# Kernel tuning notes

Hardware: AMD Instinct MI355X
Metric: run time of the kernel (lower is better)

The kernel has to match this reference:

```python
import jax, jax.numpy as jnp
import numpy as np

N, E, F, G, C, L = 20000, 320000, 75, 64, 10, 5
EPS = 1e-5


def setup_inputs():
    key = jax.random.key(0)
    ks = jax.random.split(key, 16)
    x = jax.random.normal(ks[0], (N, 6), jnp.float32)
    edge_index = jax.random.randint(ks[1], (2, E), 0, N, dtype=jnp.int32)
    batch = jnp.sort(jax.random.randint(ks[2], (N,), 0, G, dtype=jnp.int32))
    gcn_w = jax.random.normal(ks[3], (6, F), jnp.float32) / np.sqrt(6.0)
    gcn_b = jnp.zeros((F,), jnp.float32)
    pre_w = jax.random.normal(ks[4], (L, 2 * F, F), jnp.float32) / np.sqrt(2.0 * F)
    pre_b = jnp.zeros((L, F), jnp.float32)
    post_w = jax.random.normal(ks[5], (L, 13 * F, F), jnp.float32) / np.sqrt(13.0 * F)
    post_b = jnp.zeros((L, F), jnp.float32)
    lin_w = jax.random.normal(ks[6], (L, F, F), jnp.float32) / np.sqrt(1.0 * F)
    lin_b = jnp.zeros((L, F), jnp.float32)
    bn_g = jnp.ones((L, F), jnp.float32)
    bn_b = jnp.zeros((L, F), jnp.float32)
    w1 = jax.random.normal(ks[7], (F, 50), jnp.float32) / np.sqrt(1.0 * F)
    b1 = jnp.zeros((50,), jnp.float32)
    w2 = jax.random.normal(ks[8], (50, 25), jnp.float32) / np.sqrt(50.0)
    b2 = jnp.zeros((25,), jnp.float32)
    w3 = jax.random.normal(ks[9], (25, C), jnp.float32) / np.sqrt(25.0)
    b3 = jnp.zeros((C,), jnp.float32)
    return dict(x=x, edge_index=edge_index, batch=batch, gcn_w=gcn_w, gcn_b=gcn_b,
                pre_w=pre_w, pre_b=pre_b, post_w=post_w, post_b=post_b,
                lin_w=lin_w, lin_b=lin_b, bn_g=bn_g, bn_b=bn_b,
                w1=w1, b1=b1, w2=w2, b2=b2, w3=w3, b3=b3)


def reference(x, edge_index, batch, gcn_w, gcn_b, pre_w, pre_b, post_w, post_b,
              lin_w, lin_b, bn_g, bn_b, w1, b1, w2, b2, w3, b3):
    row, col = edge_index[0], edge_index[1]  # messages flow row (j) -> col (i)
    ones_e = jnp.ones((E,), jnp.float32)

    # ---- GCNConv(6, 75) with self-loops and symmetric normalization ----
    xw = x @ gcn_w                                   # [N, F]
    deg = jax.ops.segment_sum(ones_e, col, N) + 1.0  # in-degree + self-loop
    dinv = 1.0 / jnp.sqrt(deg)
    norm_e = (dinv[row] * dinv[col])[:, None]        # [E, 1]
    h = jax.ops.segment_sum(norm_e * xw[row], col, N) + (dinv * dinv)[:, None] * xw + gcn_b

    # ---- degree-based scalers (shared by all PNA layers) ----
    cnt = jax.ops.segment_sum(ones_e, col, N)        # in-degree per node
    avg_log = jnp.mean(jnp.log(cnt + 1.0))           # avg_deg['log'] from this graph's degree histogram
    d = jnp.maximum(cnt, 1.0)
    amp = (jnp.log(d + 1.0) / avg_log)[:, None]      # amplification
    att = (avg_log / jnp.log(d + 1.0))[:, None]      # attenuation
    cnt_c = jnp.maximum(cnt, 1.0)[:, None]
    has_nb = (cnt > 0)[:, None]

    for l in range(L):
        # pre-MLP on [x_i, x_j] per edge
        m = jnp.concatenate([h[col], h[row]], axis=-1) @ pre_w[l] + pre_b[l]  # [E, F]
        s = jax.ops.segment_sum(m, col, N)
        mean = s / cnt_c
        mean_sq = jax.ops.segment_sum(m * m, col, N) / cnt_c
        std = jnp.sqrt(jax.nn.relu(mean_sq - mean * mean) + EPS)
        mn = jnp.where(has_nb, jax.ops.segment_min(m, col, N), 0.0)
        mx = jnp.where(has_nb, jax.ops.segment_max(m, col, N), 0.0)
        agg = jnp.concatenate([mean, mn, mx, std], axis=-1)          # [N, 4F]
        scaled = jnp.concatenate([agg, agg * amp, agg * att], -1)    # [N, 12F]
        o = jnp.concatenate([h, scaled], axis=-1) @ post_w[l] + post_b[l]  # post-MLP
        o = o @ lin_w[l] + lin_b[l]                                  # final lin
        mu = o.mean(axis=0)
        var = o.var(axis=0)
        o = (o - mu) / jnp.sqrt(var + EPS) * bn_g[l] + bn_b[l]       # BatchNorm (batch stats)
        h = jax.nn.relu(o)

    # ---- global_add_pool + MLP (dropout = identity in eval) ----
    g = jax.ops.segment_sum(h, batch, G)
    g = jax.nn.relu(g @ w1 + b1)
    g = jax.nn.relu(g @ w2 + b2)
    return g @ w3 + b3  # [G, C]
```

## Files before the change

### kernel.cpp

```cpp
#include <hip/hip_runtime.h>
#include <hip/hip_bf16.h>

#define NN 20000
#define EE 320000
#define FF 75
#define GG 64
#define LL 5
#define EPS 1e-5f

#define KUV 96
#define NUV 160
#define KPOST 384
#define NPOST 240
#define KLIN 96
#define ASTR 392

typedef short bf16x8 __attribute__((ext_vector_type(8)));
typedef float f32x4 __attribute__((ext_vector_type(4)));

__device__ inline void gAtomicAdd(float* p, float v) { unsafeAtomicAdd(p, v); }

__device__ inline ushort f2bs(float x) {
    __hip_bfloat16 b = __float2bfloat16(x);
    return *(ushort*)&b;
}

__device__ inline float bs2f(ushort u) {
    unsigned int x = ((unsigned int)u) << 16;
    return __uint_as_float(x);
}


__global__ void count_kernel(const int* __restrict__ col, int* __restrict__ cnt, int E) {
    int e = blockIdx.x * blockDim.x + threadIdx.x;
    if (e < E) atomicAdd(&cnt[col[e]], 1);
}

__global__ void dinv_partial_kernel(const int* __restrict__ cnt, float* __restrict__ dinv,
                                    float* __restrict__ scal, int* __restrict__ bsum, int N) {
    __shared__ float red[256];
    __shared__ int redi[256];
    int tid = threadIdx.x;
    int i = blockIdx.x * 256 + tid;
    float lg = 0.f;
    int cv = 0;
    if (i < N) {
        cv = cnt[i];
        float c = (float)cv;
        dinv[i] = 1.f / sqrtf(c + 1.f);
        lg = logf(c + 1.f);
    }
    red[tid] = lg;
    redi[tid] = cv;
    __syncthreads();
    for (int s = 128; s > 0; s >>= 1) {
        if (tid < s) { red[tid] += red[tid + s]; redi[tid] += redi[tid + s]; }
        __syncthreads();
    }
    if (tid == 0) {
        gAtomicAdd(&scal[0], red[0]);
        bsum[blockIdx.x] = redi[0];
    }
}

__global__ void scanb_kernel(const int* __restrict__ bsum, int* __restrict__ bbase,
                             int* __restrict__ offs, int NB) {
    __shared__ int sh[128];
    int tid = threadIdx.x;
    int v = (tid < NB) ? bsum[tid] : 0;
    sh[tid] = v;
    __syncthreads();
    for (int d = 1; d < 128; d <<= 1) {
        int t = (tid >= d) ? sh[tid - d] : 0;
        __syncthreads();
        sh[tid] += t;
        __syncthreads();
    }
    if (tid < NB) bbase[tid] = sh[tid] - v;
    if (tid == 0) offs[NN] = EE;
}

__global__ void offs_kernel(const int* __restrict__ cnt, const int* __restrict__ bbase,
                            int* __restrict__ offs, int* __restrict__ cursor, int N) {
    __shared__ int sh[256];
    int tid = threadIdx.x;
    int i = blockIdx.x * 256 + tid;
    int v = (i < N) ? cnt[i] : 0;
    sh[tid] = v;
    __syncthreads();
    for (int d = 1; d < 256; d <<= 1) {
        int t = (tid >= d) ? sh[tid - d] : 0;
        __syncthreads();
        sh[tid] += t;
        __syncthreads();
    }
    int excl = sh[tid] - v + bbase[blockIdx.x];
    if (i < N) { offs[i] = excl; cursor[i] = excl; }
}

__global__ void fill_kernel(const int* __restrict__ row, const int* __restrict__ col,
                            int* __restrict__ cursor, int* __restrict__ csr, int E) {
    int e = blockIdx.x * blockDim.x + threadIdx.x;
    if (e < E) {
        int c = col[e];
        int pos = atomicAdd(&cursor[c], 1);
        csr[pos] = row[e];
    }
}


__global__ void xs_kernel(const float* __restrict__ x, const float* __restrict__ gw,
                          const float* __restrict__ dinv, ushort* __restrict__ xs, int N) {
    int idx = blockIdx.x * 256 + threadIdx.x;
    if (idx >= N * 80) return;
    int n = idx / 80, t = idx % 80;
    float v = 0.f;
    if (t < FF) {
        float acc = 0.f;
#pragma unroll
        for (int k = 0; k < 6; k++) acc += x[n * 6 + k] * gw[k * FF + t];
        v = dinv[n] * acc;
    }
    xs[idx] = f2bs(v);
}

__global__ __launch_bounds__(64) void gcn_kernel(
    const ushort* __restrict__ xs, const float* __restrict__ dinv,
    const int* __restrict__ offs, const int* __restrict__ csr,
    const float* __restrict__ gcn_b, const int* __restrict__ cnt,
    const float* __restrict__ scal, float* __restrict__ o2,
    float* __restrict__ amp, float* __restrict__ att, int N) {
    int i = blockIdx.x;
    int lane = threadIdx.x;
    int s0 = offs[i], s1 = offs[i + 1];
    if (lane < 40) {
        float a0 = 0.f, a1 = 0.f;
        int k = s0;
        for (; k + 1 < s1; k += 2) {
            int r0 = csr[k], r1 = csr[k + 1];
            ushort2 v0 = *(const ushort2*)(xs + (size_t)r0 * 80 + 2 * lane);
            ushort2 v1 = *(const ushort2*)(xs + (size_t)r1 * 80 + 2 * lane);
            a0 += bs2f(v0.x) + bs2f(v1.x);
            a1 += bs2f(v0.y) + bs2f(v1.y);
        }
        if (k < s1) {
            int r0 = csr[k];
            ushort2 v0 = *(const ushort2*)(xs + (size_t)r0 * 80 + 2 * lane);
            a0 += bs2f(v0.x);
            a1 += bs2f(v0.y);
        }
        ushort2 vs = *(const ushort2*)(xs + (size_t)i * 80 + 2 * lane);
        a0 += bs2f(vs.x);
        a1 += bs2f(vs.y);
        float di = dinv[i];
        int t0 = 2 * lane, t1 = 2 * lane + 1;
        if (t0 < FF) o2[(size_t)i * 80 + t0] = di * a0 + gcn_b[t0];
        if (t1 < FF) o2[(size_t)i * 80 + t1] = di * a1 + gcn_b[t1];
    } else if (lane == 63) {
        float al = scal[0] / (float)N;
        float d = fmaxf((float)cnt[i], 1.f);
        float lg = logf(d + 1.f);
        amp[i] = lg / al;
        att[i] = al / lg;
    }
}


#define S_UV (LL * NUV * KUV)
#define S_POST (LL * NPOST * KPOST)
#define S_LIN (LL * 80 * KLIN)

__global__ void prep_bt_kernel(const float* __restrict__ pre_w, const float* __restrict__ pre_b,
                               const float* __restrict__ post_w, const float* __restrict__ lin_w,
                               ushort* __restrict__ BTuv, ushort* __restrict__ BTpost,
                               ushort* __restrict__ BTlin) {
    int idx = blockIdx.x * 256 + threadIdx.x;
    if (idx < S_UV) {
        int l = idx / (NUV * KUV);
        int r = idx % (NUV * KUV);
        int c = r / KUV, k = r % KUV;
        float v = 0.f;
        if (k < FF) {
            if (c < FF) v = pre_w[((size_t)l * 150 + k) * FF + c];
            else if (c >= 80 && c < 80 + FF) v = pre_w[((size_t)l * 150 + FF + k) * FF + (c - 80)];
        } else if (k == FF && c < FF) {
            v = pre_b[l * FF + c];
        }
        BTuv[idx] = f2bs(v);
    } else if (idx < S_UV + S_POST) {
        int j = idx - S_UV;
        int l = j / (NPOST * KPOST);
        int r = j % (NPOST * KPOST);
        int c = r / KPOST, k = r % KPOST;
        float v = 0.f;
        if (k < FF) {
            if (c < FF) v = post_w[((size_t)l * 975 + k) * FF + c];
        } else if (k < 375) {
            if (c < FF) v = post_w[((size_t)l * 975 + k) * FF + c];
            else if (c >= 80 && c < 80 + FF) v = post_w[((size_t)l * 975 + k + 300) * FF + (c - 80)];
            else if (c >= 160 && c < 160 + FF) v = post_w[((size_t)l * 975 + k + 600) * FF + (c - 160)];
        }
        BTpost[j] = f2bs(v);
    } else if (idx < S_UV + S_POST + S_LIN) {
        int j = idx - S_UV - S_POST;
        int l = j / (80 * KLIN);
        int r = j % (80 * KLIN);
        int c = r / KLIN, k = r % KLIN;
        float v = (c < FF && k < FF) ? lin_w[((size_t)l * FF + k) * FF + c] : 0.f;
        BTlin[j] = f2bs(v);
    }
}


__global__ __launch_bounds__(64) void uv_bn_kernel(
    const float* __restrict__ o2, const float* __restrict__ slots,
    const float* __restrict__ bg, const float* __restrict__ bb, int apply_bn,
    const ushort* __restrict__ BT, float* __restrict__ U, ushort* __restrict__ Vb) {
    __shared__ float ssL[160];
    int lane = threadIdx.x;
    int col16 = lane & 15, quad = lane >> 4;
    int n = blockIdx.x * 16 + col16;
    const float* orow = o2 + (size_t)n * 80;
    const ushort* bbase = BT + (size_t)col16 * KUV + quad * 8;

    if (apply_bn) {
        for (int c = lane; c < 80; c += 64) {
            if (c < FF) {
                float su = 0.f, sq = 0.f;
#pragma unroll 8
                for (int s = 0; s < 32; s++) {
                    su += slots[s * 160 + c];
                    sq += slots[s * 160 + 80 + c];
                }
                float mu = su * (1.f / (float)NN);
                float var = sq * (1.f / (float)NN) - mu * mu;
                float sc = bg[c] * rsqrtf(var + EPS);
                ssL[c] = sc;
                ssL[80 + c] = bb[c] - mu * sc;
            } else {
                ssL[c] = 0.f;
                ssL[80 + c] = 0.f;
            }
        }
        __syncthreads();
    }

    f32x4 acc[10];
#pragma unroll
    for (int i = 0; i < 10; i++) acc[i] = (f32x4){0.f, 0.f, 0.f, 0.f};

#pragma unroll
    for (int kt = 0; kt < 3; kt++) {
        int kb = kt * 32 + quad * 8;
        bf16x8 af;
        if (kb < 80) {
            float4 v0 = *(const float4*)(orow + kb);
            float4 v1 = *(const float4*)(orow + kb + 4);
            float vv[8] = {v0.x, v0.y, v0.z, v0.w, v1.x, v1.y, v1.z, v1.w};
#pragma unroll
            for (int j = 0; j < 8; j++) {
                int k = kb + j;
                float v = vv[j];
                if (apply_bn) v = fmaxf(v * ssL[k] + ssL[80 + k], 0.f);
                ushort b = (k < FF) ? f2bs(v) : (k == FF ? (ushort)0x3F80 : (ushort)0);
                af[j] = (short)b;
            }
        } else {
            af = (bf16x8){0, 0, 0, 0, 0, 0, 0, 0};
        }
#pragma unroll
        for (int nt = 0; nt < 10; nt++) {
            bf16x8 bfr = *(const bf16x8*)(bbase + nt * (16 * KUV) + kt * 32);
            acc[nt] = __builtin_amdgcn_mfma_f32_16x16x32_bf16(af, bfr, acc[nt], 0, 0, 0);
        }
    }
    int n0 = blockIdx.x * 16;
#pragma unroll
    for (int nt = 0; nt < 10; nt++) {
        int col = nt * 16 + col16;
#pragma unroll
        for (int r = 0; r < 4; r++) {
            int nn = n0 + quad * 4 + r;
            if (col < FF) U[(size_t)nn * 80 + col] = acc[nt][r];
            else if (col >= 80 && col < 80 + FF) Vb[(size_t)nn * 80 + (col - 80)] = f2bs(acc[nt][r]);
        }
    }
}


__global__ __launch_bounds__(256) void agg_post_lin_kernel(
    const float* __restrict__ o2io, const float* __restrict__ slots_prev,
    const float* __restrict__ bg, const float* __restrict__ bb, int apply_bn,
    const float* __restrict__ U, const ushort* __restrict__ V,
    const int* __restrict__ offs, const int* __restrict__ csr, const int* __restrict__ cnt,
    const ushort* __restrict__ BT, const ushort* __restrict__ BL,
    const float* __restrict__ amp, const float* __restrict__ att,
    float* __restrict__ slots) {
    __shared__ float ssL[160];
    __shared__ __align__(16) ushort aggL[16 * ASTR];
    __shared__ __align__(16) ushort olds[16 * 104];
    int tid = threadIdx.x, w = tid >> 6, lane = tid & 63;
    int col16 = lane & 15, quad = lane >> 4, kseg = quad * 8;
    int n0 = blockIdx.x * 16;

    if (apply_bn) {
        for (int c = tid; c < 80; c += 256) {
            if (c < FF) {
                float su = 0.f, sq = 0.f;
#pragma unroll 8
                for (int s = 0; s < 32; s++) {
                    su += slots_prev[s * 160 + c];
                    sq += slots_prev[s * 160 + 80 + c];
                }
                float mu = su * (1.f / (float)NN);
                float var = sq * (1.f / (float)NN) - mu * mu;
                float sc = bg[c] * rsqrtf(var + EPS);
                ssL[c] = sc;
                ssL[80 + c] = bb[c] - mu * sc;
            }
        }
        __syncthreads();
    }

    for (int idx = tid; idx < 16 * 80; idx += 256) {
        int r = idx / 80, c = idx % 80;
        if (c < FF) {
            float v = o2io[(size_t)(n0 + r) * 80 + c];
            if (apply_bn) v = fmaxf(v * ssL[c] + ssL[80 + c], 0.f);
            aggL[r * ASTR + c] = f2bs(v);
        }
    }
    for (int idx = tid; idx < 16 * 9; idx += 256) {
        int r = idx / 9, c = 375 + idx % 9;
        aggL[r * ASTR + c] = 0;
    }

    for (int rr = 0; rr < 4; rr++) {
        int r = w * 4 + rr;
        int i = n0 + r;
        if (lane < 40) {
            int s0 = offs[i], s1 = offs[i + 1];
            float2 uiv = *(const float2*)(U + (size_t)i * 80 + 2 * lane);
            float ui0 = uiv.x, ui1 = uiv.y;
            float sa0 = 0.f, sq0 = 0.f, mn0 = 1e30f, mx0 = -1e30f;
            float sa1 = 0.f, sq1 = 0.f, mn1 = 1e30f, mx1 = -1e30f;
            int k = s0;
            for (; k + 1 < s1; k += 2) {
                int r0 = csr[k], r1 = csr[k + 1];
                ushort2 v0 = *(const ushort2*)(V + (size_t)r0 * 80 + 2 * lane);
                ushort2 v1 = *(const ushort2*)(V + (size_t)r1 * 80 + 2 * lane);
                float a0 = ui0 + bs2f(v0.x), b0 = ui0 + bs2f(v1.x);
                float a1 = ui1 + bs2f(v0.y), b1 = ui1 + bs2f(v1.y);
                sa0 += a0 + b0; sq0 += a0 * a0 + b0 * b0;
                mn0 = fminf(mn0, fminf(a0, b0)); mx0 = fmaxf(mx0, fmaxf(a0, b0));
                sa1 += a1 + b1; sq1 += a1 * a1 + b1 * b1;
                mn1 = fminf(mn1, fminf(a1, b1)); mx1 = fmaxf(mx1, fmaxf(a1, b1));
            }
            if (k < s1) {
                int r0 = csr[k];
                ushort2 v0 = *(const ushort2*)(V + (size_t)r0 * 80 + 2 * lane);
                float a0 = ui0 + bs2f(v0.x);
                float a1 = ui1 + bs2f(v0.y);
                sa0 += a0; sq0 += a0 * a0; mn0 = fminf(mn0, a0); mx0 = fmaxf(mx0, a0);
                sa1 += a1; sq1 += a1 * a1; mn1 = fminf(mn1, a1); mx1 = fmaxf(mx1, a1);
            }
            int c = cnt[i];
            float cc = fmaxf((float)c, 1.f);
            ushort* a = aggL + r * ASTR;
            int t0 = 2 * lane, t1 = 2 * lane + 1;
            {
                float mean = sa0 / cc;
                float stdv = sqrtf(fmaxf(sq0 / cc - mean * mean, 0.f) + EPS);
                if (c == 0) { mn0 = 0.f; mx0 = 0.f; }
                if (t0 < FF) {
                    a[75 + t0] = f2bs(mean);
                    a[150 + t0] = f2bs(mn0);
                    a[225 + t0] = f2bs(mx0);
                    a[300 + t0] = f2bs(stdv);
                }
            }
            {
                float mean = sa1 / cc;
                float stdv = sqrtf(fmaxf(sq1 / cc - mean * mean, 0.f) + EPS);
                if (c == 0) { mn1 = 0.f; mx1 = 0.f; }
                if (t1 < FF) {
                    a[75 + t1] = f2bs(mean);
                    a[150 + t1] = f2bs(mn1);
                    a[225 + t1] = f2bs(mx1);
                    a[300 + t1] = f2bs(stdv);
                }
            }
        }
    }
    __syncthreads();

    bool two_tri = (w == 0);
    f32x4 acc[6];
#pragma unroll
    for (int i = 0; i < 6; i++) acc[i] = (f32x4){0.f, 0.f, 0.f, 0.f};
#pragma unroll 2
    for (int kt = 0; kt < 12; kt++) {
        bf16x8 af = *(const bf16x8*)(aggL + col16 * ASTR + kt * 32 + kseg);
#pragma unroll
        for (int j = 0; j < 3; j++) {
            bf16x8 bfr = *(const bf16x8*)(BT + (size_t)((w + 5 * j) * 16 + col16) * KPOST + kt * 32 + kseg);
            acc[j] = __builtin_amdgcn_mfma_f32_16x16x32_bf16(af, bfr, acc[j], 0, 0, 0);
        }
        if (two_tri) {
#pragma unroll
            for (int j = 0; j < 3; j++) {
                bf16x8 bfr = *(const bf16x8*)(BT + (size_t)((4 + 5 * j) * 16 + col16) * KPOST + kt * 32 + kseg);
                acc[3 + j] = __builtin_amdgcn_mfma_f32_16x16x32_bf16(af, bfr, acc[3 + j], 0, 0, 0);
            }
        }
    }
    float ampv[4], attv[4];
#pragma unroll
    for (int r = 0; r < 4; r++) {
        int n = n0 + quad * 4 + r;
        ampv[r] = amp[n];
        attv[r] = att[n];
    }
    {
        int col = w * 16 + col16;
#pragma unroll
        for (int r = 0; r < 4; r++) {
            float ov = acc[0][r] + ampv[r] * acc[1][r] + attv[r] * acc[2][r];
            olds[(quad * 4 + r) * 104 + col] = (col < FF) ? f2bs(ov) : (ushort)0;
        }
    }
    if (two_tri) {
        int col = 64 + col16;
#pragma unroll
        for (int r = 0; r < 4; r++) {
            float ov = acc[3][r] + ampv[r] * acc[4][r] + attv[r] * acc[5][r];
            olds[(quad * 4 + r) * 104 + col] = (col < FF) ? f2bs(ov) : (ushort)0;
        }
    }
    if (w == 1) {
        *(ushort4*)(olds + (lane >> 2) * 104 + 80 + (lane & 3) * 4) = (ushort4){0, 0, 0, 0};
    }
    __syncthreads();

    f32x4 acc2[2];
    acc2[0] = (f32x4){0.f, 0.f, 0.f, 0.f};
    acc2[1] = (f32x4){0.f, 0.f, 0.f, 0.f};
#pragma unroll
    for (int kt = 0; kt < 3; kt++) {
        bf16x8 af = *(const bf16x8*)(olds + col16 * 104 + kt * 32 + kseg);
        bf16x8 b0 = *(const bf16x8*)(BL + (size_t)(w * 16 + col16) * KLIN + kt * 32 + kseg);
        acc2[0] = __builtin_amdgcn_mfma_f32_16x16x32_bf16(af, b0, acc2[0], 0, 0, 0);
        if (two_tri) {
            bf16x8 b1 = *(const bf16x8*)(BL + (size_t)(64 + col16) * KLIN + kt * 32 + kseg);
            acc2[1] = __builtin_amdgcn_mfma_f32_16x16x32_bf16(af, b1, acc2[1], 0, 0, 0);
        }
    }
    float* slot = slots + (blockIdx.x & 31) * 160;
    float* o2w = (float*)o2io;
#pragma unroll
    for (int ti = 0; ti < 2; ti++) {
        if (ti == 1 && !two_tri) break;
        int nt = (ti == 0) ? w : 4;
        int col = nt * 16 + col16;
        float s = 0.f, q = 0.f;
#pragma unroll
        for (int r = 0; r < 4; r++) {
            int n = n0 + quad * 4 + r;
            float v = acc2[ti][r];
            if (col < FF) {
                o2w[(size_t)n * 80 + col] = v;
                s += v;
                q += v * v;
            }
        }
        s += __shfl_xor(s, 16); s += __shfl_xor(s, 32);
        q += __shfl_xor(q, 16); q += __shfl_xor(q, 32);
        if (lane < 16 && col < FF) {
            gAtomicAdd(&slot[col], s);
            gAtomicAdd(&slot[80 + col], q);
        }
    }
}


__global__ void pool_kernel(const float* __restrict__ o2, const float* __restrict__ slots,
                            const float* __restrict__ bg, const float* __restrict__ bb,
                            const int* __restrict__ batch, float* __restrict__ g, int N) {
    __shared__ float acc[GG * FF];
    __shared__ float ssL[160];
    int tid = threadIdx.x;
    int n0 = blockIdx.x * 64;
    int n1 = min(n0 + 64, N);
    if (n0 >= N) return;
    for (int c = tid; c < 80; c += 256) {
        if (c < FF) {
            float su = 0.f, sq = 0.f;
#pragma unroll 8
            for (int s = 0; s < 32; s++) {
                su += slots[s * 160 + c];
                sq += slots[s * 160 + 80 + c];
            }
            float mu = su * (1.f / (float)NN);
            float var = sq * (1.f / (float)NN) - mu * mu;
            float sc = bg[c] * rsqrtf(var + EPS);
            ssL[c] = sc;
            ssL[80 + c] = bb[c] - mu * sc;
        } else {
            ssL[c] = 0.f;
            ssL[80 + c] = 0.f;
        }
    }
    int g0 = batch[n0];
    int g1 = batch[n1 - 1];
    int range = g1 - g0 + 1;
    for (int i = tid; i < range * FF; i += 256) acc[i] = 0.f;
    __syncthreads();
    int rows = n1 - n0;
    for (int idx = tid; idx < rows * FF; idx += 256) {
        int r = idx / FF, c = idx % FF;
        int n = n0 + r;
        float val = fmaxf(o2[(size_t)n * 80 + c] * ssL[c] + ssL[80 + c], 0.f);
        gAtomicAdd(&acc[(batch[n] - g0) * FF + c], val);
    }
    __syncthreads();
    for (int i = tid; i < range * FF; i += 256) gAtomicAdd(&g[g0 * FF + i], acc[i]);
}

__global__ void mlp_kernel(const float* __restrict__ g,
                           const float* __restrict__ w1, const float* __restrict__ b1,
                           const float* __restrict__ w2, const float* __restrict__ b2,
                           const float* __restrict__ w3, const float* __restrict__ b3,
                           float* __restrict__ out) {
    __shared__ float gr[FF], h1[50], h2[25];
    int gi = blockIdx.x, t = threadIdx.x;
    for (int j = t; j < FF; j += 64) gr[j] = g[gi * FF + j];
    __syncthreads();
    if (t < 50) {
        float a = b1[t];
        for (int k = 0; k < FF; k++) a += gr[k] * w1[k * 50 + t];
        h1[t] = fmaxf(a, 0.f);
    }
    __syncthreads();
    if (t < 25) {
        float a = b2[t];
        for (int k = 0; k < 50; k++) a += h1[k] * w2[k * 25 + t];
        h2[t] = fmaxf(a, 0.f);
    }
    __syncthreads();
    if (t < 10) {
        float a = b3[t];
        for (int k = 0; k < 25; k++) a += h2[k] * w3[k * 10 + t];
        out[gi * 10 + t] = a;
    }
}


extern "C" void kernel_launch(void* const* d_in, const int* in_sizes, int n_in,
                              void* d_out, int out_size, void* d_ws, size_t ws_size,
                              hipStream_t stream) {
    const float* x = (const float*)d_in[0];
    const int* ei = (const int*)d_in[1];
    const int* batch = (const int*)d_in[2];
    const float* gcn_w = (const float*)d_in[3];
    const float* gcn_b = (const float*)d_in[4];
    const float* pre_w = (const float*)d_in[5];
    const float* pre_b = (const float*)d_in[6];
    const float* post_w = (const float*)d_in[7];
    const float* lin_w = (const float*)d_in[9];
    const float* bn_g = (const float*)d_in[11];
    const float* bn_b = (const float*)d_in[12];
    const float* w1 = (const float*)d_in[13];
    const float* b1 = (const float*)d_in[14];
    const float* w2 = (const float*)d_in[15];
    const float* b2 = (const float*)d_in[16];
    const float* w3 = (const float*)d_in[17];
    const float* b3 = (const float*)d_in[18];
    float* out = (float*)d_out;

    const int* row = ei;
    const int* col = ei + EE;

    char* ws = (char*)d_ws;
    size_t off = 0;
    auto alloc = [&](size_t bytes) {
        char* p = ws + off;
        off += (bytes + 255) & ~(size_t)255;
        return p;
    };
    int* cnt = (int*)alloc(NN * 4);
    int* offs = (int*)alloc((NN + 1) * 4);
    int* cursor = (int*)alloc(NN * 4);
    int* csr = (int*)alloc(EE * 4);
    int* bsum = (int*)alloc(128 * 4);
    int* bbase = (int*)alloc(128 * 4);
    float* dinv = (float*)alloc(NN * 4);
    float* amp = (float*)alloc(NN * 4);
    float* att = (float*)alloc(NN * 4);
    float* scal = (float*)alloc((1 + LL * 32 * 160) * 4);
    float* slotbase = scal + 1;
    float* o2 = (float*)alloc((size_t)NN * 80 * 4);
    float* ubuf = (float*)alloc((size_t)NN * 80 * 4);
    ushort* vbuf = (ushort*)alloc((size_t)NN * 80 * 2);
    ushort* BTuv = (ushort*)alloc((size_t)S_UV * 2);
    ushort* BTpost = (ushort*)alloc((size_t)S_POST * 2);
    ushort* BTlin = (ushort*)alloc((size_t)S_LIN * 2);
    float* gbuf = (float*)alloc(GG * FF * 4);

    hipMemsetAsync(cnt, 0, NN * 4, stream);
    hipMemsetAsync(scal, 0, (1 + LL * 32 * 160) * 4, stream);
    hipMemsetAsync(gbuf, 0, GG * FF * 4, stream);

    const int B = 256;
    const int NB = (NN + 255) / 256;
    count_kernel<<<(EE + B - 1) / B, B, 0, stream>>>(col, cnt, EE);
    dinv_partial_kernel<<<NB, B, 0, stream>>>(cnt, dinv, scal, bsum, NN);
    scanb_kernel<<<1, 128, 0, stream>>>(bsum, bbase, offs, NB);
    offs_kernel<<<NB, B, 0, stream>>>(cnt, bbase, offs, cursor, NN);
    fill_kernel<<<(EE + B - 1) / B, B, 0, stream>>>(row, col, cursor, csr, EE);
    xs_kernel<<<(NN * 80 + B - 1) / B, B, 0, stream>>>(x, gcn_w, dinv, vbuf, NN);
    gcn_kernel<<<NN, 64, 0, stream>>>(vbuf, dinv, offs, csr, gcn_b, cnt, scal,
                                      o2, amp, att, NN);
    {
        int tot = S_UV + S_POST + S_LIN;
        prep_bt_kernel<<<(tot + B - 1) / B, B, 0, stream>>>(pre_w, pre_b, post_w, lin_w,
                                                            BTuv, BTpost, BTlin);
    }

    const int GS = NN / 16;
    for (int l = 0; l < LL; l++) {
        float* slots_prev = slotbase + (l - 1) * 32 * 160;
        float* slots = slotbase + l * 32 * 160;
        int lp = (l > 0) ? (l - 1) : 0;
        int ab = (l > 0) ? 1 : 0;
        const float* sp = (l == 0) ? slotbase : slots_prev;

        uv_bn_kernel<<<GS, 64, 0, stream>>>(o2, sp, bn_g + lp * FF, bn_b + lp * FF, ab,
                                            BTuv + (size_t)l * NUV * KUV, ubuf, vbuf);
        agg_post_lin_kernel<<<GS, 256, 0, stream>>>(
            o2, sp, bn_g + lp * FF, bn_b + lp * FF, ab, ubuf, vbuf, offs, csr, cnt,
            BTpost + (size_t)l * NPOST * KPOST, BTlin + (size_t)l * 80 * KLIN,
            amp, att, slots);
    }

    pool_kernel<<<(NN + 63) / 64, 256, 0, stream>>>(o2, slotbase + (LL - 1) * 32 * 160,
                                                    bn_g + (LL - 1) * FF, bn_b + (LL - 1) * FF,
                                                    batch, gbuf, NN);
    mlp_kernel<<<GG, 64, 0, stream>>>(gbuf, w1, b1, w2, b2, w3, b3, out);
}
```

Baseline: 536.2 us.

## Split edge aggregation into its own per-node kernel and widen uv kernel

The fused aggregate+post+lin kernel is split in two. A per-node edge_agg kernel (one 64-thread block per node) writes mean/min/max/std into a global bf16 staging buffer, and a separate post_lin kernel reads its A operand from that buffer instead of shared memory. The uv kernel now uses four waves that divide the ten output tiles, and wave 0 also writes the BN'd h into the staging buffer. This raises parallelism for the irregular gather, which was serialized four nodes per wave. The cost is an extra launch per layer and a global round trip of about 15 MB per layer.

Measured after the change: 535.3 us. No clear change (-0.2%).

```diff
diff --git a/kernel.cpp b/kernel.cpp
--- a/kernel.cpp
+++ b/kernel.cpp
@@ -13,7 +13,6 @@
 #define KPOST 384
 #define NPOST 240
 #define KLIN 96
-#define ASTR 392
 
 typedef short bf16x8 __attribute__((ext_vector_type(8)));
 typedef float f32x4 __attribute__((ext_vector_type(4)));
@@ -212,19 +211,21 @@
 }
 
 
-__global__ __launch_bounds__(64) void uv_bn_kernel(
+__global__ __launch_bounds__(256) void uv_bn_kernel(
     const float* __restrict__ o2, const float* __restrict__ slots,
     const float* __restrict__ bg, const float* __restrict__ bb, int apply_bn,
-    const ushort* __restrict__ BT, float* __restrict__ U, ushort* __restrict__ Vb) {
+    const ushort* __restrict__ BT, float* __restrict__ U, ushort* __restrict__ Vb,
+    ushort* __restrict__ hagg) {
     __shared__ float ssL[160];
-    int lane = threadIdx.x;
+    int tid = threadIdx.x, w = tid >> 6, lane = tid & 63;
     int col16 = lane & 15, quad = lane >> 4;
     int n = blockIdx.x * 16 + col16;
     const float* orow = o2 + (size_t)n * 80;
     const ushort* bbase = BT + (size_t)col16 * KUV + quad * 8;
 
     if (apply_bn) {
-        for (int c = lane; c < 80; c += 64) {
+        if (tid < 80) {
+            int c = tid;
             if (c < FF) {
                 float su = 0.f, sq = 0.f;
 #pragma unroll 8
@@ -245,9 +246,13 @@
         __syncthreads();
     }
 
-    f32x4 acc[10];
-#pragma unroll
-    for (int i = 0; i < 10; i++) acc[i] = (f32x4){0.f, 0.f, 0.f, 0.f};
+    const int tstart[4] = {0, 3, 5, 8};
+    const int tcnt[4] = {3, 2, 3, 2};
+    int t0 = tstart[w], tc = tcnt[w];
+
+    f32x4 acc[3];
+#pragma unroll
+    for (int i = 0; i < 3; i++) acc[i] = (f32x4){0.f, 0.f, 0.f, 0.f};
 
 #pragma unroll
     for (int kt = 0; kt < 3; kt++) {
@@ -265,142 +270,49 @@
                 ushort b = (k < FF) ? f2bs(v) : (k == FF ? (ushort)0x3F80 : (ushort)0);
                 af[j] = (short)b;
             }
+            if (w == 0 && kb < FF) {
+                *(bf16x8*)(hagg + (size_t)n * KPOST + kb) = af;
+            }
         } else {
             af = (bf16x8){0, 0, 0, 0, 0, 0, 0, 0};
         }
-#pragma unroll
-        for (int nt = 0; nt < 10; nt++) {
-            bf16x8 bfr = *(const bf16x8*)(bbase + nt * (16 * KUV) + kt * 32);
-            acc[nt] = __builtin_amdgcn_mfma_f32_16x16x32_bf16(af, bfr, acc[nt], 0, 0, 0);
+        for (int j = 0; j < tc; j++) {
+            bf16x8 bfr = *(const bf16x8*)(bbase + (t0 + j) * (16 * KUV) + kt * 32);
+            acc[j] = __builtin_amdgcn_mfma_f32_16x16x32_bf16(af, bfr, acc[j], 0, 0, 0);
         }
     }
     int n0 = blockIdx.x * 16;
-#pragma unroll
-    for (int nt = 0; nt < 10; nt++) {
-        int col = nt * 16 + col16;
+    for (int j = 0; j < tc; j++) {
+        int col = (t0 + j) * 16 + col16;
 #pragma unroll
         for (int r = 0; r < 4; r++) {
             int nn = n0 + quad * 4 + r;
-            if (col < FF) U[(size_t)nn * 80 + col] = acc[nt][r];
-            else if (col >= 80 && col < 80 + FF) Vb[(size_t)nn * 80 + (col - 80)] = f2bs(acc[nt][r]);
-        }
-    }
-}
-
-
-__global__ __launch_bounds__(256) void agg_post_lin_kernel(
-    const float* __restrict__ o2io, const float* __restrict__ slots_prev,
-    const float* __restrict__ bg, const float* __restrict__ bb, int apply_bn,
-    const float* __restrict__ U, const ushort* __restrict__ V,
-    const int* __restrict__ offs, const int* __restrict__ csr, const int* __restrict__ cnt,
-    const ushort* __restrict__ BT, const ushort* __restrict__ BL,
-    const float* __restrict__ amp, const float* __restrict__ att,
+            if (col < FF) U[(size_t)nn * 80 + col] = acc[j][r];
+            else if (col >= 80 && col < 80 + FF) Vb[(size_t)nn * 80 + (col - 80)] = f2bs(acc[j][r]);
+        }
+    }
+}
+
+
+__global__ __launch_bounds__(256) void post_lin_kernel(
+    const ushort* __restrict__ A, const ushort* __restrict__ BT,
+    const ushort* __restrict__ BL, const float* __restrict__ amp,
+    const float* __restrict__ att, float* __restrict__ o2,
     float* __restrict__ slots) {
-    __shared__ float ssL[160];
-    __shared__ __align__(16) ushort aggL[16 * ASTR];
     __shared__ __align__(16) ushort olds[16 * 104];
     int tid = threadIdx.x, w = tid >> 6, lane = tid & 63;
     int col16 = lane & 15, quad = lane >> 4, kseg = quad * 8;
     int n0 = blockIdx.x * 16;
-
-    if (apply_bn) {
-        for (int c = tid; c < 80; c += 256) {
-            if (c < FF) {
-                float su = 0.f, sq = 0.f;
-#pragma unroll 8
-                for (int s = 0; s < 32; s++) {
-                    su += slots_prev[s * 160 + c];
-                    sq += slots_prev[s * 160 + 80 + c];
-                }
-                float mu = su * (1.f / (float)NN);
-                float var = sq * (1.f / (float)NN) - mu * mu;
-                float sc = bg[c] * rsqrtf(var + EPS);
-                ssL[c] = sc;
-                ssL[80 + c] = bb[c] - mu * sc;
-            }
-        }
-        __syncthreads();
-    }
-
-    for (int idx = tid; idx < 16 * 80; idx += 256) {
-        int r = idx / 80, c = idx % 80;
-        if (c < FF) {
-            float v = o2io[(size_t)(n0 + r) * 80 + c];
-            if (apply_bn) v = fmaxf(v * ssL[c] + ssL[80 + c], 0.f);
-            aggL[r * ASTR + c] = f2bs(v);
-        }
-    }
-    for (int idx = tid; idx < 16 * 9; idx += 256) {
-        int r = idx / 9, c = 375 + idx % 9;
-        aggL[r * ASTR + c] = 0;
-    }
-
-    for (int rr = 0; rr < 4; rr++) {
-        int r = w * 4 + rr;
-        int i = n0 + r;
-        if (lane < 40) {
-            int s0 = offs[i], s1 = offs[i + 1];
-            float2 uiv = *(const float2*)(U + (size_t)i * 80 + 2 * lane);
-            float ui0 = uiv.x, ui1 = uiv.y;
-            float sa0 = 0.f, sq0 = 0.f, mn0 = 1e30f, mx0 = -1e30f;
-            float sa1 = 0.f, sq1 = 0.f, mn1 = 1e30f, mx1 = -1e30f;
-            int k = s0;
-            for (; k + 1 < s1; k += 2) {
-                int r0 = csr[k], r1 = csr[k + 1];
-                ushort2 v0 = *(const ushort2*)(V + (size_t)r0 * 80 + 2 * lane);
-                ushort2 v1 = *(const ushort2*)(V + (size_t)r1 * 80 + 2 * lane);
-                float a0 = ui0 + bs2f(v0.x), b0 = ui0 + bs2f(v1.x);
-                float a1 = ui1 + bs2f(v0.y), b1 = ui1 + bs2f(v1.y);
-                sa0 += a0 + b0; sq0 += a0 * a0 + b0 * b0;
-                mn0 = fminf(mn0, fminf(a0, b0)); mx0 = fmaxf(mx0, fmaxf(a0, b0));
-                sa1 += a1 + b1; sq1 += a1 * a1 + b1 * b1;
-                mn1 = fminf(mn1, fminf(a1, b1)); mx1 = fmaxf(mx1, fmaxf(a1, b1));
-            }
-            if (k < s1) {
-                int r0 = csr[k];
-                ushort2 v0 = *(const ushort2*)(V + (size_t)r0 * 80 + 2 * lane);
-                float a0 = ui0 + bs2f(v0.x);
-                float a1 = ui1 + bs2f(v0.y);
-                sa0 += a0; sq0 += a0 * a0; mn0 = fminf(mn0, a0); mx0 = fmaxf(mx0, a0);
-                sa1 += a1; sq1 += a1 * a1; mn1 = fminf(mn1, a1); mx1 = fmaxf(mx1, a1);
-            }
-            int c = cnt[i];
-            float cc = fmaxf((float)c, 1.f);
-            ushort* a = aggL + r * ASTR;
-            int t0 = 2 * lane, t1 = 2 * lane + 1;
-            {
-                float mean = sa0 / cc;
-                float stdv = sqrtf(fmaxf(sq0 / cc - mean * mean, 0.f) + EPS);
-                if (c == 0) { mn0 = 0.f; mx0 = 0.f; }
-                if (t0 < FF) {
-                    a[75 + t0] = f2bs(mean);
-                    a[150 + t0] = f2bs(mn0);
-                    a[225 + t0] = f2bs(mx0);
-                    a[300 + t0] = f2bs(stdv);
-                }
-            }
-            {
-                float mean = sa1 / cc;
-                float stdv = sqrtf(fmaxf(sq1 / cc - mean * mean, 0.f) + EPS);
-                if (c == 0) { mn1 = 0.f; mx1 = 0.f; }
-                if (t1 < FF) {
-                    a[75 + t1] = f2bs(mean);
-                    a[150 + t1] = f2bs(mn1);
-                    a[225 + t1] = f2bs(mx1);
-                    a[300 + t1] = f2bs(stdv);
-                }
-            }
-        }
-    }
-    __syncthreads();
-
+    const ushort* arow = A + (size_t)(n0 + col16) * KPOST + kseg;
     bool two_tri = (w == 0);
+
     f32x4 acc[6];
 #pragma unroll
     for (int i = 0; i < 6; i++) acc[i] = (f32x4){0.f, 0.f, 0.f, 0.f};
+
 #pragma unroll 2
     for (int kt = 0; kt < 12; kt++) {
-        bf16x8 af = *(const bf16x8*)(aggL + col16 * ASTR + kt * 32 + kseg);
+        bf16x8 af = *(const bf16x8*)(arow + kt * 32);
 #pragma unroll
         for (int j = 0; j < 3; j++) {
             bf16x8 bfr = *(const bf16x8*)(BT + (size_t)((w + 5 * j) * 16 + col16) * KPOST + kt * 32 + kseg);
@@ -456,7 +368,6 @@
         }
     }
     float* slot = slots + (blockIdx.x & 31) * 160;
-    float* o2w = (float*)o2io;
 #pragma unroll
     for (int ti = 0; ti < 2; ti++) {
         if (ti == 1 && !two_tri) break;
@@ -468,7 +379,7 @@
             int n = n0 + quad * 4 + r;
             float v = acc2[ti][r];
             if (col < FF) {
-                o2w[(size_t)n * 80 + col] = v;
+                o2[(size_t)n * 80 + col] = v;
                 s += v;
                 q += v * v;
             }
@@ -479,6 +390,70 @@
             gAtomicAdd(&slot[col], s);
             gAtomicAdd(&slot[80 + col], q);
         }
+    }
+}
+
+
+__global__ __launch_bounds__(64) void edge_agg_kernel(
+    const float* __restrict__ U, const ushort* __restrict__ V,
+    const int* __restrict__ offs, const int* __restrict__ csr,
+    const int* __restrict__ cnt, ushort* __restrict__ hagg) {
+    int i = blockIdx.x;
+    int lane = threadIdx.x;
+    int s0 = offs[i], s1 = offs[i + 1];
+    if (lane < 40) {
+        float2 uiv = *(const float2*)(U + (size_t)i * 80 + 2 * lane);
+        float ui0 = uiv.x, ui1 = uiv.y;
+        float sa0 = 0.f, sq0 = 0.f, mn0 = 1e30f, mx0 = -1e30f;
+        float sa1 = 0.f, sq1 = 0.f, mn1 = 1e30f, mx1 = -1e30f;
+        int k = s0;
+        for (; k + 1 < s1; k += 2) {
+            int r0 = csr[k], r1 = csr[k + 1];
+            ushort2 v0 = *(const ushort2*)(V + (size_t)r0 * 80 + 2 * lane);
+            ushort2 v1 = *(const ushort2*)(V + (size_t)r1 * 80 + 2 * lane);
+            float a0 = ui0 + bs2f(v0.x), b0 = ui0 + bs2f(v1.x);
+            float a1 = ui1 + bs2f(v0.y), b1 = ui1 + bs2f(v1.y);
+            sa0 += a0 + b0; sq0 += a0 * a0 + b0 * b0;
+            mn0 = fminf(mn0, fminf(a0, b0)); mx0 = fmaxf(mx0, fmaxf(a0, b0));
+            sa1 += a1 + b1; sq1 += a1 * a1 + b1 * b1;
+            mn1 = fminf(mn1, fminf(a1, b1)); mx1 = fmaxf(mx1, fmaxf(a1, b1));
+        }
+        if (k < s1) {
+            int r0 = csr[k];
+            ushort2 v0 = *(const ushort2*)(V + (size_t)r0 * 80 + 2 * lane);
+            float a0 = ui0 + bs2f(v0.x);
+            float a1 = ui1 + bs2f(v0.y);
+            sa0 += a0; sq0 += a0 * a0; mn0 = fminf(mn0, a0); mx0 = fmaxf(mx0, a0);
+            sa1 += a1; sq1 += a1 * a1; mn1 = fminf(mn1, a1); mx1 = fmaxf(mx1, a1);
+        }
+        int c = cnt[i];
+        float cc = fmaxf((float)c, 1.f);
+        ushort* a = hagg + (size_t)i * KPOST + FF;
+        int t0 = 2 * lane, t1 = 2 * lane + 1;
+        {
+            float mean = sa0 / cc;
+            float stdv = sqrtf(fmaxf(sq0 / cc - mean * mean, 0.f) + EPS);
+            if (c == 0) { mn0 = 0.f; mx0 = 0.f; }
+            if (t0 < FF) {
+                a[t0] = f2bs(mean);
+                a[FF + t0] = f2bs(mn0);
+                a[2 * FF + t0] = f2bs(mx0);
+                a[3 * FF + t0] = f2bs(stdv);
+            }
+        }
+        {
+            float mean = sa1 / cc;
+            float stdv = sqrtf(fmaxf(sq1 / cc - mean * mean, 0.f) + EPS);
+            if (c == 0) { mn1 = 0.f; mx1 = 0.f; }
+            if (t1 < FF) {
+                a[t1] = f2bs(mean);
+                a[FF + t1] = f2bs(mn1);
+                a[2 * FF + t1] = f2bs(mx1);
+                a[3 * FF + t1] = f2bs(stdv);
+            }
+        }
+    } else if (lane >= 48 && lane < 57) {
+        hagg[(size_t)i * KPOST + 375 + (lane - 48)] = 0;
     }
 }
 
@@ -601,6 +576,7 @@
     float* o2 = (float*)alloc((size_t)NN * 80 * 4);
     float* ubuf = (float*)alloc((size_t)NN * 80 * 4);
     ushort* vbuf = (ushort*)alloc((size_t)NN * 80 * 2);
+    ushort* hagg = (ushort*)alloc((size_t)NN * KPOST * 2);
     ushort* BTuv = (ushort*)alloc((size_t)S_UV * 2);
     ushort* BTpost = (ushort*)alloc((size_t)S_POST * 2);
     ushort* BTlin = (ushort*)alloc((size_t)S_LIN * 2);
@@ -634,12 +610,12 @@
         int ab = (l > 0) ? 1 : 0;
         const float* sp = (l == 0) ? slotbase : slots_prev;
 
-        uv_bn_kernel<<<GS, 64, 0, stream>>>(o2, sp, bn_g + lp * FF, bn_b + lp * FF, ab,
-                                            BTuv + (size_t)l * NUV * KUV, ubuf, vbuf);
-        agg_post_lin_kernel<<<GS, 256, 0, stream>>>(
-            o2, sp, bn_g + lp * FF, bn_b + lp * FF, ab, ubuf, vbuf, offs, csr, cnt,
-            BTpost + (size_t)l * NPOST * KPOST, BTlin + (size_t)l * 80 * KLIN,
-            amp, att, slots);
+        uv_bn_kernel<<<GS, 256, 0, stream>>>(o2, sp, bn_g + lp * FF, bn_b + lp * FF, ab,
+                                             BTuv + (size_t)l * NUV * KUV, ubuf, vbuf, hagg);
+        edge_agg_kernel<<<NN, 64, 0, stream>>>(ubuf, vbuf, offs, csr, cnt, hagg);
+        post_lin_kernel<<<GS, 256, 0, stream>>>(hagg, BTpost + (size_t)l * NPOST * KPOST,
+                                                BTlin + (size_t)l * 80 * KLIN, amp, att,
+                                                o2, slots);
     }
 
     pool_kernel<<<(NN + 63) / 64, 256, 0, stream>>>(o2, slotbase + (LL - 1) * 32 * 160,
```
